# Performance work log

Measured on AMD Instinct MI355X. Metric: run time of the kernel, lower is better.

Reference implementation:

```python
import jax, jax.numpy as jnp
import numpy as np

P = 4  # polynomial kernel degree


def setup_inputs() -> dict:
    key = jax.random.key(0)
    k1, k2, k3, k4 = jax.random.split(key, 4)
    m, n, d = 16384, 8192, 64
    x_p = jax.random.normal(k1, (m, d), dtype=jnp.float32)
    X = jax.random.normal(k2, (n, d), dtype=jnp.float32)
    alpha = jax.random.uniform(k3, (n,), dtype=jnp.float32, minval=0.0, maxval=0.2)
    b = jax.random.uniform(k4, (1,), dtype=jnp.float32, minval=0.0, maxval=0.2)
    return {"x_p": x_p, "X": X, "alpha": alpha, "b": b}


def reference(x_p, X, alpha, b):
    # SVR prediction with polynomial kernel, vectorized:
    # f(x_p) = sum_i alpha_i * (1 + x_p . X_i)^P + b
    # x_p: [m, d], X: [n, d] -> K: [m, n]
    K = (1.0 + jnp.einsum('md,nd->mn', x_p, X)) ** P
    return K @ alpha + b  # [m]
```

## Files before the change

kernel.cpp:

```cpp
#include <hip/hip_runtime.h>
#include <hip/hip_bf16.h>
#include <stdint.h>


typedef __attribute__((ext_vector_type(8))) short bf16x8;
typedef __attribute__((ext_vector_type(8))) unsigned short ushort8;
typedef __attribute__((ext_vector_type(4))) float f32x4;
typedef __attribute__((ext_vector_type(2))) float f32v2;

#define MM 16384
#define NN 8192
#define DD 64
#define NSPLIT 4
#define CHUNK 64
#define CHUNKS_PER_BLK 32
#define BM 128
#define MT 8

__device__ __forceinline__ unsigned short f2bf(float f) {
    uint32_t u = __float_as_uint(f);
    uint32_t r = (u + 0x7FFFu + ((u >> 16) & 1u)) >> 16;
    return (unsigned short)r;
}

__device__ __forceinline__ void gll16(const void* g, void* l) {
    __builtin_amdgcn_global_load_lds(
        (const __attribute__((address_space(1))) unsigned int*)g,
        (__attribute__((address_space(3))) unsigned int*)l, 16, 0, 0);
}

__global__ void convert_kernel(const float* __restrict__ xp,
                               const float* __restrict__ X,
                               const float* __restrict__ alpha,
                               unsigned short* __restrict__ xbf,
                               unsigned short* __restrict__ Xs,
                               float* __restrict__ alpha4f) {
    const int xp4 = MM * DD / 4;
    const int xu = NN * DD / 8;
    const int tot = xp4 + xu;
    int tid0 = blockIdx.x * blockDim.x + threadIdx.x;
    if (tid0 < NN) alpha4f[tid0] = sqrtf(sqrtf(alpha[tid0]));
    int stride = gridDim.x * blockDim.x;
    for (int i = tid0; i < tot; i += stride) {
        if (i < xp4) {
            float4 v = ((const float4*)xp)[i];
            ushort4 o;
            o.x = f2bf(v.x); o.y = f2bf(v.y); o.z = f2bf(v.z); o.w = f2bf(v.w);
            *(ushort4*)(xbf + (size_t)i * 4) = o;
        } else {
            int u = i - xp4;
            int n = u >> 3;
            int slot = u & 7;
            float a4 = sqrtf(sqrtf(alpha[n]));
            float4 va = ((const float4*)X)[n * 16 + slot * 2];
            float4 vb = ((const float4*)X)[n * 16 + slot * 2 + 1];
            ushort8 o;
            o[0] = f2bf(va.x * a4); o[1] = f2bf(va.y * a4);
            o[2] = f2bf(va.z * a4); o[3] = f2bf(va.w * a4);
            o[4] = f2bf(vb.x * a4); o[5] = f2bf(vb.y * a4);
            o[6] = f2bf(vb.z * a4); o[7] = f2bf(vb.w * a4);
            size_t dst = (size_t)(n >> 6) * 4096 + (n & 63) * 64
                       + ((slot ^ (n & 7)) * 8);
            *(ushort8*)(Xs + dst) = o;
        }
    }
}


#define STAGE(CL)                                                         \
    {                                                                     \
        const char* gs = (const char*)Xs                                  \
            + (size_t)(chunk0 + (CL)) * 8192 + w * 2048 + lane * 16;      \
        char* lb = smem + w * 4096 + ((CL) & 1) * 2048;                   \
        gll16(gs, lb);                                                    \
        gll16(gs + 1024, lb + 1024);                                      \
    }

__global__ __launch_bounds__(256, 2) void svr_main(
        const unsigned short* __restrict__ xbf,
        const unsigned short* __restrict__ Xs,
        const float* __restrict__ alpha4f,
        float* __restrict__ partials) {
    __shared__ char smem[26624];
    const int tid  = threadIdx.x;
    const int lane = tid & 63;
    const int w    = tid >> 6;
    const int r    = lane & 15;
    const int g    = lane >> 4;
    const int mgroup = blockIdx.x >> 2;
    const int ns     = blockIdx.x & 3;
    const int chunk0 = ns * CHUNKS_PER_BLK;

    bf16x8 a[MT][2];
#pragma unroll
    for (int mt = 0; mt < MT; ++mt)
#pragma unroll
        for (int ks = 0; ks < 2; ++ks)
            a[mt][ks] = *(const bf16x8*)(
                xbf + (size_t)(mgroup * BM + mt * 16 + r) * DD
                    + ks * 32 + g * 8);

    {
        const char* ga = (const char*)(alpha4f + chunk0 * CHUNK)
                       + w * 2048 + lane * 16;
        char* la = smem + 16384 + w * 2048;
        gll16(ga, la);
        gll16(ga + 1024, la + 1024);
    }
    STAGE(0);
    __syncthreads();

    f32v2 red2[MT][2];
#pragma unroll
    for (int mt = 0; mt < MT; ++mt) {
        red2[mt][0] = (f32v2){0.f, 0.f};
        red2[mt][1] = (f32v2){0.f, 0.f};
    }

    const float* alpha_lds = (const float*)(smem + 16384);

#pragma unroll 1
    for (int c = 0; c < CHUNKS_PER_BLK; ++c) {
        if (c + 1 < CHUNKS_PER_BLK) {
            STAGE(c + 1);
            asm volatile("s_waitcnt vmcnt(2)" ::: "memory");
        } else {
            asm volatile("s_waitcnt vmcnt(0)" ::: "memory");
        }
        __builtin_amdgcn_sched_barrier(0);
        const char* rowp = smem + w * 4096 + (c & 1) * 2048 + r * 128;
        bf16x8 b0 = *(const bf16x8*)(rowp + ((g ^ (r & 7)) * 16));
        bf16x8 b1 = *(const bf16x8*)(rowp + (((4 + g) ^ (r & 7)) * 16));
        float av = alpha_lds[c * CHUNK + w * 16 + r];
        f32x4 cav = (f32x4){av, av, av, av};
        f32x4 acc[MT];
        __builtin_amdgcn_s_setprio(1);
#pragma unroll
        for (int mt = 0; mt < MT; ++mt)
            acc[mt] = __builtin_amdgcn_mfma_f32_16x16x32_bf16(
                a[mt][0], b0, cav, 0, 0, 0);
#pragma unroll
        for (int mt = 0; mt < MT; ++mt)
            acc[mt] = __builtin_amdgcn_mfma_f32_16x16x32_bf16(
                a[mt][1], b1, acc[mt], 0, 0, 0);
        __builtin_amdgcn_s_setprio(0);
#pragma unroll
        for (int mt = 0; mt < MT; ++mt) {
            f32v2 lo = (f32v2){acc[mt][0], acc[mt][1]};
            f32v2 hi = (f32v2){acc[mt][2], acc[mt][3]};
            f32v2 lo2 = lo * lo;
            f32v2 hi2 = hi * hi;
            red2[mt][0] = lo2 * lo2 + red2[mt][0];
            red2[mt][1] = hi2 * hi2 + red2[mt][1];
        }
    }

    float* sred = (float*)(smem + 24576);
#pragma unroll
    for (int mt = 0; mt < MT; ++mt)
#pragma unroll
        for (int i = 0; i < 4; ++i) {
            float v = red2[mt][i >> 1][i & 1];
            v += __shfl_xor(v, 1);
            v += __shfl_xor(v, 2);
            v += __shfl_xor(v, 4);
            v += __shfl_xor(v, 8);
            if (r == 0) sred[w * BM + mt * 16 + g * 4 + i] = v;
        }
    __syncthreads();
    if (tid < BM) {
        float s = sred[tid] + sred[BM + tid] + sred[2 * BM + tid]
                + sred[3 * BM + tid];
        partials[(size_t)ns * MM + mgroup * BM + tid] = s;
    }
}

__global__ void finalize_kernel(const float* __restrict__ partials,
                                const float* __restrict__ bbias,
                                float* __restrict__ out) {
    int m = blockIdx.x * blockDim.x + threadIdx.x;
    if (m < MM) {
        float s = bbias[0];
#pragma unroll
        for (int c = 0; c < NSPLIT; ++c) s += partials[(size_t)c * MM + m];
        out[m] = s;
    }
}

extern "C" void kernel_launch(void* const* d_in, const int* in_sizes, int n_in,
                              void* d_out, int out_size, void* d_ws, size_t ws_size,
                              hipStream_t stream) {
    const float* xp    = (const float*)d_in[0];
    const float* X     = (const float*)d_in[1];
    const float* alpha = (const float*)d_in[2];
    const float* b     = (const float*)d_in[3];
    float* out = (float*)d_out;

    unsigned short* xbf = (unsigned short*)d_ws;
    unsigned short* Xs  = xbf + (size_t)MM * DD;
    float* alpha4f = (float*)(Xs + (size_t)NN * DD);
    float* partials = alpha4f + NN;

    hipLaunchKernelGGL(convert_kernel, dim3(1280), dim3(256), 0, stream,
                       xp, X, alpha, xbf, Xs, alpha4f);

    hipLaunchKernelGGL(svr_main, dim3(128 * NSPLIT), dim3(256), 0, stream,
                       xbf, Xs, alpha4f, partials);

    hipLaunchKernelGGL(finalize_kernel, dim3(MM / 256), dim3(256), 0, stream,
                       partials, b, out);
}
```

Measured before the change: 34.99 us.

## Halve M tile, raise occupancy, and triple-buffer X chunk prefetch

Cuts each block's M tile from 128 to 64 rows, which doubles the grid to 1024 blocks and raises the launch-bounds occupancy target to 4 blocks per CU. The double-buffered LDS staging of X chunks becomes a three-slot ring with prefetch distance two. Prefetches past the end wrap to already-loaded chunks so the vmcnt(4) wait count stays uniform, at the cost of a few redundant loads. The aim is more waves to hide latency and deeper load/compute overlap, but each block now gets less reuse of the B tile, doing half as many MFMAs per staged chunk.

```diff
diff --git a/kernel.cpp b/kernel.cpp
--- a/kernel.cpp
+++ b/kernel.cpp
@@ -13,9 +13,9 @@
 #define DD 64
 #define NSPLIT 4
 #define CHUNK 64
-#define CHUNKS_PER_BLK 32
-#define BM 128
-#define MT 8
+#define CPB 32
+#define BM 64
+#define MT 4
 
 __device__ __forceinline__ unsigned short f2bf(float f) {
     uint32_t u = __float_as_uint(f);
@@ -67,21 +67,12 @@
 }
 
 
-#define STAGE(CL)                                                         \
-    {                                                                     \
-        const char* gs = (const char*)Xs                                  \
-            + (size_t)(chunk0 + (CL)) * 8192 + w * 2048 + lane * 16;      \
-        char* lb = smem + w * 4096 + ((CL) & 1) * 2048;                   \
-        gll16(gs, lb);                                                    \
-        gll16(gs + 1024, lb + 1024);                                      \
-    }
-
-__global__ __launch_bounds__(256, 2) void svr_main(
+__global__ __launch_bounds__(256, 4) void svr_main(
         const unsigned short* __restrict__ xbf,
         const unsigned short* __restrict__ Xs,
         const float* __restrict__ alpha4f,
         float* __restrict__ partials) {
-    __shared__ char smem[26624];
+    __shared__ char smem[33792];
     const int tid  = threadIdx.x;
     const int lane = tid & 63;
     const int w    = tid >> 6;
@@ -89,7 +80,7 @@
     const int g    = lane >> 4;
     const int mgroup = blockIdx.x >> 2;
     const int ns     = blockIdx.x & 3;
-    const int chunk0 = ns * CHUNKS_PER_BLK;
+    const int chunk0 = ns * CPB;
 
     bf16x8 a[MT][2];
 #pragma unroll
@@ -103,11 +94,18 @@
     {
         const char* ga = (const char*)(alpha4f + chunk0 * CHUNK)
                        + w * 2048 + lane * 16;
-        char* la = smem + 16384 + w * 2048;
+        char* la = smem + 24576 + w * 2048;
         gll16(ga, la);
         gll16(ga + 1024, la + 1024);
     }
-    STAGE(0);
+#pragma unroll
+    for (int j = 0; j < 2; ++j) {
+        const char* gs = (const char*)Xs
+            + (size_t)(chunk0 + j) * 8192 + w * 2048 + lane * 16;
+        char* lb = smem + w * 6144 + j * 2048;
+        gll16(gs, lb);
+        gll16(gs + 1024, lb + 1024);
+    }
     __syncthreads();
 
     f32v2 red2[MT][2];
@@ -117,21 +115,25 @@
         red2[mt][1] = (f32v2){0.f, 0.f};
     }
 
-    const float* alpha_lds = (const float*)(smem + 16384);
+    const float* alda = (const float*)(smem + 24576);
 
 #pragma unroll 1
-    for (int c = 0; c < CHUNKS_PER_BLK; ++c) {
-        if (c + 1 < CHUNKS_PER_BLK) {
-            STAGE(c + 1);
-            asm volatile("s_waitcnt vmcnt(2)" ::: "memory");
-        } else {
-            asm volatile("s_waitcnt vmcnt(0)" ::: "memory");
-        }
+    for (int c = 0; c < CPB; ++c) {
+        {
+            const int cs = c + 2;
+            const int src = (cs < CPB) ? cs : cs - CPB;
+            const char* gs = (const char*)Xs
+                + (size_t)(chunk0 + src) * 8192 + w * 2048 + lane * 16;
+            char* lb = smem + w * 6144 + (cs % 3) * 2048;
+            gll16(gs, lb);
+            gll16(gs + 1024, lb + 1024);
+        }
+        asm volatile("s_waitcnt vmcnt(4)" ::: "memory");
         __builtin_amdgcn_sched_barrier(0);
-        const char* rowp = smem + w * 4096 + (c & 1) * 2048 + r * 128;
+        const char* rowp = smem + w * 6144 + (c % 3) * 2048 + r * 128;
         bf16x8 b0 = *(const bf16x8*)(rowp + ((g ^ (r & 7)) * 16));
         bf16x8 b1 = *(const bf16x8*)(rowp + (((4 + g) ^ (r & 7)) * 16));
-        float av = alpha_lds[c * CHUNK + w * 16 + r];
+        float av = alda[c * CHUNK + w * 16 + r];
         f32x4 cav = (f32x4){av, av, av, av};
         f32x4 acc[MT];
         __builtin_amdgcn_s_setprio(1);
@@ -155,7 +157,7 @@
         }
     }
 
-    float* sred = (float*)(smem + 24576);
+    float* sred = (float*)(smem + 32768);
 #pragma unroll
     for (int mt = 0; mt < MT; ++mt)
 #pragma unroll
@@ -204,7 +206,7 @@
     hipLaunchKernelGGL(convert_kernel, dim3(1280), dim3(256), 0, stream,
                        xp, X, alpha, xbf, Xs, alpha4f);
 
-    hipLaunchKernelGGL(svr_main, dim3(128 * NSPLIT), dim3(256), 0, stream,
+    hipLaunchKernelGGL(svr_main, dim3((MM / BM) * NSPLIT), dim3(256), 0, stream,
                        xbf, Xs, alpha4f, partials);
 
     hipLaunchKernelGGL(finalize_kernel, dim3(MM / 256), dim3(256), 0, stream,
```

After: 35.86 us. 1.02x slower.
